# Optimization experiments

Hardware: AMD Instinct MI355X
Metric: run time of the kernel (lower is better)

## Reference

```python
import jax, jax.numpy as jnp
import numpy as np

N_NODES = 50000
N_EDGES = 800000
F_IN = 512
H1 = 64
H2 = 128
N_CLASSES = 10
N_GRAPHS = 64


def _sage_conv(x, src, dst, w_l, b_l, w_r, n_nodes):
    # mean-aggregate neighbor features (messages flow src -> dst), then
    # out = lin_l(mean_neigh) + lin_r(x)   (PyG SAGEConv defaults)
    msg = x[src]                                           # [E, F] gather
    agg = jax.ops.segment_sum(msg, dst, num_segments=n_nodes)
    deg = jax.ops.segment_sum(jnp.ones((src.shape[0], 1), x.dtype), dst,
                              num_segments=n_nodes)
    mean = agg / jnp.maximum(deg, 1.0)                     # 0 for isolated nodes
    return mean @ w_l + b_l + x @ w_r


def setup_inputs() -> dict:
    key = jax.random.key(0)
    ks = jax.random.split(key, 12)
    x = jax.random.normal(ks[0], (N_NODES, F_IN), dtype=jnp.float32)
    edge_index = jax.random.randint(ks[1], (2, N_EDGES), 0, N_NODES, dtype=jnp.int64)
    batch = jnp.sort(jax.random.randint(ks[2], (N_NODES,), 0, N_GRAPHS, dtype=jnp.int64))

    def glorot(k, fan_in, fan_out):
        s = jnp.sqrt(6.0 / (fan_in + fan_out)).astype(jnp.float32)
        return jax.random.uniform(k, (fan_in, fan_out), jnp.float32, -s, s)

    return {
        "x": x, "edge_index": edge_index, "batch": batch,
        "w1_l": glorot(ks[3], F_IN, H1), "b1_l": jnp.zeros((H1,), jnp.float32),
        "w1_r": glorot(ks[4], F_IN, H1),
        "w2_l": glorot(ks[5], H1, H2), "b2_l": jnp.zeros((H2,), jnp.float32),
        "w2_r": glorot(ks[6], H1, H2),
        "w_fc": glorot(ks[7], H2, N_CLASSES),
        "b_fc": jnp.zeros((N_CLASSES,), jnp.float32),
    }


def reference(x, edge_index, batch, w1_l, b1_l, w1_r, w2_l, b2_l, w2_r, w_fc, b_fc):
    src, dst = edge_index[0], edge_index[1]
    n = x.shape[0]
    h = jax.nn.relu(_sage_conv(x, src, dst, w1_l, b1_l, w1_r, n))
    # dropout is identity in eval mode
    h = _sage_conv(h, src, dst, w2_l, b2_l, w2_r, n)        # [N, H2]
    # global mean pool over graphs
    summed = jax.ops.segment_sum(h, batch, num_segments=N_GRAPHS)
    cnt = jax.ops.segment_sum(jnp.ones((n, 1), h.dtype), batch, num_segments=N_GRAPHS)
    pooled = summed / jnp.maximum(cnt, 1.0)                 # [G, H2]
    logits = pooled @ w_fc + b_fc                           # [G, C]
    return jax.nn.log_softmax(logits, axis=1)
```

## Files before the change

### kernel.cpp

```cpp
#include <hip/hip_runtime.h>

#define NN 50000
#define NE 800000
#define FIN 512
#define H1DIM 64
#define H2DIM 128
#define NC 10
#define NG 64
#define NRT 3125

typedef __attribute__((ext_vector_type(8))) short bf16x8;
typedef __attribute__((ext_vector_type(4))) float f32x4;

__device__ inline short f2bf(float f) {
  unsigned u = __float_as_uint(f);
  unsigned r = u + 0x7fffu + ((u >> 16) & 1u);
  return (short)(r >> 16);
}
__device__ inline float bf2f(short s) {
  return __uint_as_float(((unsigned)(unsigned short)s) << 16);
}

__global__ __launch_bounds__(256) void xbf_prep_kernel(
    const float* __restrict__ x, short* __restrict__ xbf) {
  int w = blockIdx.x * 4 + (threadIdx.x >> 6);
  int lane = threadIdx.x & 63;
  int rt = w >> 4;
  int ks = w & 15;
  int row = rt * 16 + (lane & 15);
  int k = ks * 32 + (lane >> 4) * 8;
  const float* p = x + (size_t)row * FIN + k;
  float4 v0 = *(const float4*)(p);
  float4 v1 = *(const float4*)(p + 4);
  bf16x8 o;
  o[0] = f2bf(v0.x); o[1] = f2bf(v0.y); o[2] = f2bf(v0.z); o[3] = f2bf(v0.w);
  o[4] = f2bf(v1.x); o[5] = f2bf(v1.y); o[6] = f2bf(v1.z); o[7] = f2bf(v1.w);
  *(bf16x8*)(xbf + ((size_t)w * 64 + lane) * 8) = o;
}

__global__ __launch_bounds__(256) void wbtf_prep_kernel(
    const float* __restrict__ wl, const float* __restrict__ wr,
    short* __restrict__ wbtf) {
  int w = blockIdx.x * 4 + (threadIdx.x >> 6);
  int lane = threadIdx.x & 63;
  int ni = w >> 4;
  int ks = w & 15;
  int n = ni * 16 + (lane & 15);
  int k = ks * 32 + (lane >> 4) * 8;
  bf16x8 o;
#pragma unroll
  for (int j = 0; j < 8; j++) {
    float v = (n < 64) ? wl[(size_t)(k + j) * 64 + n]
                       : wr[(size_t)(k + j) * 64 + (n - 64)];
    o[j] = f2bf(v);
  }
  *(bf16x8*)(wbtf + ((size_t)w * 64 + lane) * 8) = o;
}

__global__ __launch_bounds__(256) void gemm1_mfma_kernel(
    const short* __restrict__ xbf, const short* __restrict__ wbtf,
    short* __restrict__ xwl, float* __restrict__ xwr) {
  int w = blockIdx.x * 4 + (threadIdx.x >> 6);
  int lane = threadIdx.x & 63;
  int rt0 = w * 2;
  int rt1 = rt0 + 1;
  if (rt0 >= NRT) return;
  bool ok1 = (rt1 < NRT);
  int rt1c = ok1 ? rt1 : rt0;

  const size_t la = (size_t)lane * 8;
  const short* pa0 = xbf + (size_t)rt0 * 8192 + la;
  const short* pa1 = xbf + (size_t)rt1c * 8192 + la;
  const short* pb = wbtf + la;

  const f32x4 z = {0.f, 0.f, 0.f, 0.f};
  f32x4 acc[2][8];
#pragma unroll
  for (int mi = 0; mi < 2; mi++)
#pragma unroll
    for (int ni = 0; ni < 8; ni++) acc[mi][ni] = z;

  bf16x8 A0[2], A1[2], B0[8], B1[8];
  A0[0] = *(const bf16x8*)(pa0);
  A0[1] = *(const bf16x8*)(pa1);
#pragma unroll
  for (int ni = 0; ni < 8; ni++)
    B0[ni] = *(const bf16x8*)(pb + (size_t)ni * 8192);

#pragma unroll
  for (int ks = 0; ks < 16; ks += 2) {
    if (ks + 1 < 16) {
      A1[0] = *(const bf16x8*)(pa0 + (ks + 1) * 512);
      A1[1] = *(const bf16x8*)(pa1 + (ks + 1) * 512);
#pragma unroll
      for (int ni = 0; ni < 8; ni++)
        B1[ni] = *(const bf16x8*)(pb + (size_t)ni * 8192 + (ks + 1) * 512);
    }
#pragma unroll
    for (int mi = 0; mi < 2; mi++)
#pragma unroll
      for (int ni = 0; ni < 8; ni++)
        acc[mi][ni] = __builtin_amdgcn_mfma_f32_16x16x32_bf16(
            A0[mi], B0[ni], acc[mi][ni], 0, 0, 0);
    if (ks + 2 < 16) {
      A0[0] = *(const bf16x8*)(pa0 + (ks + 2) * 512);
      A0[1] = *(const bf16x8*)(pa1 + (ks + 2) * 512);
#pragma unroll
      for (int ni = 0; ni < 8; ni++)
        B0[ni] = *(const bf16x8*)(pb + (size_t)ni * 8192 + (ks + 2) * 512);
    }
#pragma unroll
    for (int mi = 0; mi < 2; mi++)
#pragma unroll
      for (int ni = 0; ni < 8; ni++)
        acc[mi][ni] = __builtin_amdgcn_mfma_f32_16x16x32_bf16(
            A1[mi], B1[ni], acc[mi][ni], 0, 0, 0);
  }

  int q = lane >> 4;
  int l15 = lane & 15;
#pragma unroll
  for (int mi = 0; mi < 2; mi++) {
    if (mi == 1 && !ok1) break;
    int row_base = (mi ? rt1 : rt0) * 16 + q * 4;
#pragma unroll
    for (int ni = 0; ni < 8; ni++) {
      int col = ni * 16 + l15;
      int c = col & 63;
#pragma unroll
      for (int r = 0; r < 4; r++) {
        int row = row_base + r;
        if (col < 64) xwl[(size_t)row * 64 + c] = f2bf(acc[mi][ni][r]);
        else          xwr[(size_t)row * 64 + c] = acc[mi][ni][r];
      }
    }
  }
}

__global__ __launch_bounds__(256) void hist_kernel(const int* __restrict__ dst,
                                                   int* __restrict__ cnt) {
  int i = (blockIdx.x * 256 + threadIdx.x) * 4;
  if (i < NE) {
    int4 d = *(const int4*)(dst + i);
    atomicAdd(&cnt[d.x], 1);
    atomicAdd(&cnt[d.y], 1);
    atomicAdd(&cnt[d.z], 1);
    atomicAdd(&cnt[d.w], 1);
  }
}

#define SCAN_BLOCKS 196

__global__ __launch_bounds__(256) void scan1_kernel(const int* __restrict__ cnt,
                                                    int* __restrict__ excl,
                                                    int* __restrict__ bsum) {
  __shared__ int s[256];
  int t = threadIdx.x;
  int i = blockIdx.x * 256 + t;
  int v = (i < NN) ? cnt[i] : 0;
  s[t] = v;
  __syncthreads();
  for (int off = 1; off < 256; off <<= 1) {
    int u = (t >= off) ? s[t - off] : 0;
    __syncthreads();
    s[t] += u;
    __syncthreads();
  }
  if (i < NN) excl[i] = s[t] - v;
  if (t == 255) bsum[blockIdx.x] = s[255];
}

__global__ __launch_bounds__(256) void scan2_kernel(int* __restrict__ bsum) {
  __shared__ int s[256];
  int t = threadIdx.x;
  int v = (t < SCAN_BLOCKS) ? bsum[t] : 0;
  s[t] = v;
  __syncthreads();
  for (int off = 1; off < 256; off <<= 1) {
    int u = (t >= off) ? s[t - off] : 0;
    __syncthreads();
    s[t] += u;
    __syncthreads();
  }
  bsum[t] = s[t] - v;
}

__global__ __launch_bounds__(256) void scan3_kernel(const int* __restrict__ bsum,
                                                    int* __restrict__ rowptr,
                                                    int* __restrict__ cursor) {
  int t = threadIdx.x;
  int i = blockIdx.x * 256 + t;
  if (i < NN) {
    int p = rowptr[i] + bsum[blockIdx.x];
    rowptr[i] = p;
    cursor[i] = p;
  }
  if (i == 0) rowptr[NN] = NE;
}

__global__ __launch_bounds__(256) void scatter_kernel(
    const int* __restrict__ src, const int* __restrict__ dst,
    int* __restrict__ cursor, int* __restrict__ ssrc) {
  int i = (blockIdx.x * 256 + threadIdx.x) * 4;
  if (i < NE) {
    int4 s = *(const int4*)(src + i);
    int4 d = *(const int4*)(dst + i);
    int p0 = atomicAdd(&cursor[d.x], 1); ssrc[p0] = s.x;
    int p1 = atomicAdd(&cursor[d.y], 1); ssrc[p1] = s.y;
    int p2 = atomicAdd(&cursor[d.z], 1); ssrc[p2] = s.z;
    int p3 = atomicAdd(&cursor[d.w], 1); ssrc[p3] = s.w;
  }
}

__global__ __launch_bounds__(256) void agg1_h1_kernel(
    const int* __restrict__ rowptr, const int* __restrict__ ssrc,
    const short* __restrict__ xwl, const float* __restrict__ xwr,
    const float* __restrict__ b1, short* __restrict__ h1) {
  int node = blockIdx.x * 4 + (threadIdx.x >> 6);
  if (node >= NN) return;
  int lane = threadIdx.x & 63;
  int c = lane & 7;
  int r = lane >> 3;
  int lo = rowptr[node], hi = rowptr[node + 1];
  float acc[8];
#pragma unroll
  for (int k = 0; k < 8; k++) acc[k] = 0.f;
  for (int e = lo + r; e < hi; e += 8) {
    int s = ssrc[e];
    bf16x8 v = *(const bf16x8*)(xwl + (size_t)s * 64 + c * 8);
#pragma unroll
    for (int k = 0; k < 8; k++) acc[k] += bf2f(v[k]);
  }
#pragma unroll
  for (int k = 0; k < 8; k++) {
    acc[k] += __shfl_xor(acc[k], 8);
    acc[k] += __shfl_xor(acc[k], 16);
    acc[k] += __shfl_xor(acc[k], 32);
  }
  if (r == 0) {
    float dg = fmaxf((float)(hi - lo), 1.0f);
    const float* xr = xwr + (size_t)node * 64 + c * 8;
    bf16x8 out;
#pragma unroll
    for (int k = 0; k < 8; k++) {
      float v = fmaxf(acc[k] / dg + b1[c * 8 + k] + xr[k], 0.f);
      out[k] = f2bf(v);
    }
    *(bf16x8*)(h1 + (size_t)node * 64 + c * 8) = out;
  }
}

__global__ __launch_bounds__(256) void agg2_kernel(
    const int* __restrict__ rowptr, const int* __restrict__ ssrc,
    const short* __restrict__ h1, float* __restrict__ agg2) {
  int node = blockIdx.x * 4 + (threadIdx.x >> 6);
  if (node >= NN) return;
  int lane = threadIdx.x & 63;
  int c = lane & 7;
  int r = lane >> 3;
  int lo = rowptr[node], hi = rowptr[node + 1];
  float acc[8];
#pragma unroll
  for (int k = 0; k < 8; k++) acc[k] = 0.f;
  for (int e = lo + r; e < hi; e += 8) {
    int s = ssrc[e];
    bf16x8 v = *(const bf16x8*)(h1 + (size_t)s * 64 + c * 8);
#pragma unroll
    for (int k = 0; k < 8; k++) acc[k] += bf2f(v[k]);
  }
#pragma unroll
  for (int k = 0; k < 8; k++) {
    acc[k] += __shfl_xor(acc[k], 8);
    acc[k] += __shfl_xor(acc[k], 16);
    acc[k] += __shfl_xor(acc[k], 32);
  }
  if (r == 0) {
    float* p = agg2 + (size_t)node * 64 + c * 8;
    f32x4 lo4 = {acc[0], acc[1], acc[2], acc[3]};
    f32x4 hi4 = {acc[4], acc[5], acc[6], acc[7]};
    *(f32x4*)(p) = lo4;
    *(f32x4*)(p + 4) = hi4;
  }
}

__global__ __launch_bounds__(256) void pool1_kernel(
    const int* __restrict__ batch, const float* __restrict__ agg2,
    const short* __restrict__ h1, const int* __restrict__ rowptr,
    float* __restrict__ poolA, float* __restrict__ poolB,
    float* __restrict__ poolCnt) {
  int t = threadIdx.x;
  int c = t & 15;
  int s = t >> 4;
  int n0 = blockIdx.x * 256 + s * 16;
  int n1 = n0 + 16;
  if (n1 > NN) n1 = NN;

  f32x4 aA = {0.f, 0.f, 0.f, 0.f};
  f32x4 aB = {0.f, 0.f, 0.f, 0.f};
  int cur_g = -1;
  float run = 0.f;
  for (int n = n0; n < n1; n++) {
    int g = batch[n];
    if (g != cur_g) {
      if (cur_g >= 0) {
        float* pa = poolA + (size_t)cur_g * 64 + c * 4;
        float* pb = poolB + (size_t)cur_g * 64 + c * 4;
#pragma unroll
        for (int k = 0; k < 4; k++) {
          atomicAdd(&pa[k], aA[k]);
          atomicAdd(&pb[k], aB[k]);
        }
        if (c == 0) atomicAdd(&poolCnt[cur_g], run);
      }
      cur_g = g;
      aA = (f32x4){0.f, 0.f, 0.f, 0.f};
      aB = (f32x4){0.f, 0.f, 0.f, 0.f};
      run = 0.f;
    }
    float rd = 1.0f / fmaxf((float)(rowptr[n + 1] - rowptr[n]), 1.0f);
    f32x4 a2 = *(const f32x4*)(agg2 + (size_t)n * 64 + c * 4);
    const short* hp = h1 + (size_t)n * 64 + c * 4;
#pragma unroll
    for (int k = 0; k < 4; k++) {
      aA[k] = fmaf(a2[k], rd, aA[k]);
      aB[k] += bf2f(hp[k]);
    }
    run += 1.f;
  }
  if (cur_g >= 0) {
    float* pa = poolA + (size_t)cur_g * 64 + c * 4;
    float* pb = poolB + (size_t)cur_g * 64 + c * 4;
#pragma unroll
    for (int k = 0; k < 4; k++) {
      atomicAdd(&pa[k], aA[k]);
      atomicAdd(&pb[k], aB[k]);
    }
    if (c == 0) atomicAdd(&poolCnt[cur_g], run);
  }
}

__global__ __launch_bounds__(128) void final_kernel(
    const float* __restrict__ poolA, const float* __restrict__ poolB,
    const float* __restrict__ poolCnt, const float* __restrict__ w2l,
    const float* __restrict__ w2r, const float* __restrict__ b2,
    const float* __restrict__ wfc, const float* __restrict__ bfc,
    float* __restrict__ out) {
  int g = blockIdx.x;
  int j = threadIdx.x;
  __shared__ float sp[H2DIM];
  __shared__ float sl[NC];

  float invc = 1.0f / fmaxf(poolCnt[g], 1.0f);
  float v = b2[j];
  for (int k = 0; k < 64; k++) {
    float a = poolA[g * 64 + k] * invc;
    float b = poolB[g * 64 + k] * invc;
    v = fmaf(a, w2l[k * 128 + j], v);
    v = fmaf(b, w2r[k * 128 + j], v);
  }
  sp[j] = v;
  __syncthreads();
  if (j < NC) {
    float lg = bfc[j];
    for (int k = 0; k < H2DIM; k++) lg = fmaf(sp[k], wfc[k * NC + j], lg);
    sl[j] = lg;
  }
  __syncthreads();
  if (j < NC) {
    float m = -1e30f;
    for (int k = 0; k < NC; k++) m = fmaxf(m, sl[k]);
    float s = 0.f;
    for (int k = 0; k < NC; k++) s += expf(sl[k] - m);
    out[g * NC + j] = sl[j] - m - logf(s);
  }
}

extern "C" void kernel_launch(void* const* d_in, const int* in_sizes, int n_in,
                              void* d_out, int out_size, void* d_ws,
                              size_t ws_size, hipStream_t stream) {
  const float* x   = (const float*)d_in[0];
  const int* edge  = (const int*)d_in[1];
  const int* batch = (const int*)d_in[2];
  const float* w1l = (const float*)d_in[3];
  const float* b1l = (const float*)d_in[4];
  const float* w1r = (const float*)d_in[5];
  const float* w2l = (const float*)d_in[6];
  const float* b2l = (const float*)d_in[7];
  const float* w2r = (const float*)d_in[8];
  const float* wfc = (const float*)d_in[9];
  const float* bfc = (const float*)d_in[10];
  float* out = (float*)d_out;

  const int* src = edge;
  const int* dst = edge + NE;

  const size_t NF = (size_t)NN * 64;
  int*   cnt     = (int*)d_ws;
  float* poolA   = (float*)(cnt + NN);
  float* poolB   = poolA + (size_t)NG * 64;
  float* poolCnt = poolB + (size_t)NG * 64;
  int*   cursor  = (int*)(poolCnt + NG);
  int*   rowptr  = cursor + NN;
  int*   ssrc    = rowptr + 50004;
  int*   bsum    = ssrc + NE;
  short* xbf     = (short*)(bsum + 256);
  short* xwl     = xbf + (size_t)NN * 512;
  short* h1s     = xwl + NF;
  short* wbtf    = h1s + NF;
  float* xwr     = (float*)(wbtf + 65536);
  float* agg2    = xwr + NF;

  hipMemsetAsync(cnt, 0, (NN + 2 * NG * 64 + NG) * sizeof(int), stream);

  hist_kernel<<<(NE / 4 + 255) / 256, 256, 0, stream>>>(dst, cnt);
  scan1_kernel<<<SCAN_BLOCKS, 256, 0, stream>>>(cnt, rowptr, bsum);
  scan2_kernel<<<1, 256, 0, stream>>>(bsum);
  scan3_kernel<<<SCAN_BLOCKS, 256, 0, stream>>>(bsum, rowptr, cursor);
  scatter_kernel<<<(NE / 4 + 255) / 256, 256, 0, stream>>>(src, dst, cursor, ssrc);

  xbf_prep_kernel<<<(NRT * 16) / 4, 256, 0, stream>>>(x, xbf);
  wbtf_prep_kernel<<<32, 256, 0, stream>>>(w1l, w1r, wbtf);
  gemm1_mfma_kernel<<<(NRT / 2 + 4) / 4, 256, 0, stream>>>(xbf, wbtf, xwl, xwr);

  agg1_h1_kernel<<<(NN + 3) / 4, 256, 0, stream>>>(rowptr, ssrc, xwl, xwr, b1l, h1s);
  agg2_kernel<<<(NN + 3) / 4, 256, 0, stream>>>(rowptr, ssrc, h1s, agg2);
  pool1_kernel<<<SCAN_BLOCKS, 256, 0, stream>>>(batch, agg2, h1s, rowptr, poolA, poolB, poolCnt);
  final_kernel<<<NG, 128, 0, stream>>>(poolA, poolB, poolCnt, w2l, w2r, b2l, wfc, bfc, out);
}
```

Measured before the change: 366.5 us.

## Fuse CSR build into one grid-barrier kernel and convert x to bf16 inside GEMM

Replaces the hist/scan1/scan2/scan3/scatter launches with a single persistent sort kernel of 196 blocks. Its phases are separated by an atomic-counter grid barrier, and it zeroes the counts itself instead of relying on the memset. The separate x-to-bf16 prep pass is removed: the GEMM now loads fp32 x directly and converts in registers, and each wave handles one row tile instead of two. This saves several launches and one full read/write of the bf16 copy of x, but the grid barrier depends on all 196 blocks being co-resident, and the GEMM reads twice as many bytes of A per tile.

```diff
diff --git a/kernel.cpp b/kernel.cpp
--- a/kernel.cpp
+++ b/kernel.cpp
@@ -8,6 +8,8 @@
 #define NC 10
 #define NG 64
 #define NRT 3125
+#define SB 196
+#define SORT_THREADS (SB * 256)
 
 typedef __attribute__((ext_vector_type(8))) short bf16x8;
 typedef __attribute__((ext_vector_type(4))) float f32x4;
@@ -21,21 +23,79 @@
   return __uint_as_float(((unsigned)(unsigned short)s) << 16);
 }
 
-__global__ __launch_bounds__(256) void xbf_prep_kernel(
-    const float* __restrict__ x, short* __restrict__ xbf) {
-  int w = blockIdx.x * 4 + (threadIdx.x >> 6);
-  int lane = threadIdx.x & 63;
-  int rt = w >> 4;
-  int ks = w & 15;
-  int row = rt * 16 + (lane & 15);
-  int k = ks * 32 + (lane >> 4) * 8;
-  const float* p = x + (size_t)row * FIN + k;
-  float4 v0 = *(const float4*)(p);
-  float4 v1 = *(const float4*)(p + 4);
-  bf16x8 o;
-  o[0] = f2bf(v0.x); o[1] = f2bf(v0.y); o[2] = f2bf(v0.z); o[3] = f2bf(v0.w);
-  o[4] = f2bf(v1.x); o[5] = f2bf(v1.y); o[6] = f2bf(v1.z); o[7] = f2bf(v1.w);
-  *(bf16x8*)(xbf + ((size_t)w * 64 + lane) * 8) = o;
+__device__ __forceinline__ void gbar(int* bar, int id) {
+  __syncthreads();
+  if (threadIdx.x == 0) {
+    __threadfence();
+    atomicAdd(&bar[id], 1);
+    while (atomicAdd(&bar[id], 0) < SB) {}
+  }
+  __syncthreads();
+}
+
+__global__ __launch_bounds__(256) void sort_kernel(
+    const int* __restrict__ src, const int* __restrict__ dst,
+    int* __restrict__ cnt, int* __restrict__ rowptr, int* __restrict__ cursor,
+    int* __restrict__ bsum, int* __restrict__ ssrc, int* __restrict__ bar) {
+  const int b = blockIdx.x;
+  const int t = threadIdx.x;
+  const int idx = b * 256 + t;
+  __shared__ int s[256];
+
+  {
+    int i = ((b + 98) % SB) * 256 + t;
+    if (i < NN) cnt[i] = 0;
+  }
+  gbar(bar, 0);
+
+  for (int j = idx; j < NE / 4; j += SORT_THREADS) {
+    int4 d = *(const int4*)(dst + j * 4);
+    atomicAdd(&cnt[d.x], 1);
+    atomicAdd(&cnt[d.y], 1);
+    atomicAdd(&cnt[d.z], 1);
+    atomicAdd(&cnt[d.w], 1);
+  }
+  gbar(bar, 1);
+
+  int v = (idx < NN) ? atomicAdd(&cnt[idx], 0) : 0;
+  s[t] = v;
+  __syncthreads();
+  for (int off = 1; off < 256; off <<= 1) {
+    int u = (t >= off) ? s[t - off] : 0;
+    __syncthreads();
+    s[t] += u;
+    __syncthreads();
+  }
+  if (idx < NN) rowptr[idx] = s[t] - v;
+  if (t == 255) bsum[b] = s[255];
+  gbar(bar, 2);
+
+  int bv = (t < SB) ? atomicAdd(&bsum[t], 0) : 0;
+  s[t] = bv;
+  __syncthreads();
+  for (int off = 1; off < 256; off <<= 1) {
+    int u = (t >= off) ? s[t - off] : 0;
+    __syncthreads();
+    s[t] += u;
+    __syncthreads();
+  }
+  int prefix = (b == 0) ? 0 : s[b - 1];
+  if (idx < NN) {
+    int p = rowptr[idx] + prefix;
+    rowptr[idx] = p;
+    cursor[idx] = p;
+  }
+  if (idx == 0) rowptr[NN] = NE;
+  gbar(bar, 3);
+
+  for (int j = idx; j < NE / 4; j += SORT_THREADS) {
+    int4 sv = *(const int4*)(src + j * 4);
+    int4 dv = *(const int4*)(dst + j * 4);
+    int p0 = atomicAdd(&cursor[dv.x], 1); ssrc[p0] = sv.x;
+    int p1 = atomicAdd(&cursor[dv.y], 1); ssrc[p1] = sv.y;
+    int p2 = atomicAdd(&cursor[dv.z], 1); ssrc[p2] = sv.z;
+    int p3 = atomicAdd(&cursor[dv.w], 1); ssrc[p3] = sv.w;
+  }
 }
 
 __global__ __launch_bounds__(256) void wbtf_prep_kernel(
@@ -57,32 +117,26 @@
   *(bf16x8*)(wbtf + ((size_t)w * 64 + lane) * 8) = o;
 }
 
-__global__ __launch_bounds__(256) void gemm1_mfma_kernel(
-    const short* __restrict__ xbf, const short* __restrict__ wbtf,
+__global__ __launch_bounds__(256) void gemm1_kernel(
+    const float* __restrict__ x, const short* __restrict__ wbtf,
     short* __restrict__ xwl, float* __restrict__ xwr) {
   int w = blockIdx.x * 4 + (threadIdx.x >> 6);
+  if (w >= NRT) return;
   int lane = threadIdx.x & 63;
-  int rt0 = w * 2;
-  int rt1 = rt0 + 1;
-  if (rt0 >= NRT) return;
-  bool ok1 = (rt1 < NRT);
-  int rt1c = ok1 ? rt1 : rt0;
-
-  const size_t la = (size_t)lane * 8;
-  const short* pa0 = xbf + (size_t)rt0 * 8192 + la;
-  const short* pa1 = xbf + (size_t)rt1c * 8192 + la;
-  const short* pb = wbtf + la;
+  int l15 = lane & 15;
+  int q = lane >> 4;
+  const float* px = x + (size_t)(w * 16 + l15) * FIN + q * 8;
+  const short* pb = wbtf + (size_t)lane * 8;
 
   const f32x4 z = {0.f, 0.f, 0.f, 0.f};
-  f32x4 acc[2][8];
-#pragma unroll
-  for (int mi = 0; mi < 2; mi++)
-#pragma unroll
-    for (int ni = 0; ni < 8; ni++) acc[mi][ni] = z;
-
-  bf16x8 A0[2], A1[2], B0[8], B1[8];
-  A0[0] = *(const bf16x8*)(pa0);
-  A0[1] = *(const bf16x8*)(pa1);
+  f32x4 acc[8];
+#pragma unroll
+  for (int ni = 0; ni < 8; ni++) acc[ni] = z;
+
+  float4 av0, av1, nv0, nv1;
+  bf16x8 B0[8], B1[8];
+  av0 = *(const float4*)(px);
+  av1 = *(const float4*)(px + 4);
 #pragma unroll
   for (int ni = 0; ni < 8; ni++)
     B0[ni] = *(const bf16x8*)(pb + (size_t)ni * 8192);
@@ -90,125 +144,52 @@
 #pragma unroll
   for (int ks = 0; ks < 16; ks += 2) {
     if (ks + 1 < 16) {
-      A1[0] = *(const bf16x8*)(pa0 + (ks + 1) * 512);
-      A1[1] = *(const bf16x8*)(pa1 + (ks + 1) * 512);
+      nv0 = *(const float4*)(px + (ks + 1) * 32);
+      nv1 = *(const float4*)(px + (ks + 1) * 32 + 4);
 #pragma unroll
       for (int ni = 0; ni < 8; ni++)
         B1[ni] = *(const bf16x8*)(pb + (size_t)ni * 8192 + (ks + 1) * 512);
     }
-#pragma unroll
-    for (int mi = 0; mi < 2; mi++)
+    {
+      bf16x8 af;
+      af[0] = f2bf(av0.x); af[1] = f2bf(av0.y);
+      af[2] = f2bf(av0.z); af[3] = f2bf(av0.w);
+      af[4] = f2bf(av1.x); af[5] = f2bf(av1.y);
+      af[6] = f2bf(av1.z); af[7] = f2bf(av1.w);
 #pragma unroll
       for (int ni = 0; ni < 8; ni++)
-        acc[mi][ni] = __builtin_amdgcn_mfma_f32_16x16x32_bf16(
-            A0[mi], B0[ni], acc[mi][ni], 0, 0, 0);
+        acc[ni] = __builtin_amdgcn_mfma_f32_16x16x32_bf16(af, B0[ni], acc[ni], 0, 0, 0);
+    }
     if (ks + 2 < 16) {
-      A0[0] = *(const bf16x8*)(pa0 + (ks + 2) * 512);
-      A0[1] = *(const bf16x8*)(pa1 + (ks + 2) * 512);
+      av0 = *(const float4*)(px + (ks + 2) * 32);
+      av1 = *(const float4*)(px + (ks + 2) * 32 + 4);
 #pragma unroll
       for (int ni = 0; ni < 8; ni++)
         B0[ni] = *(const bf16x8*)(pb + (size_t)ni * 8192 + (ks + 2) * 512);
     }
-#pragma unroll
-    for (int mi = 0; mi < 2; mi++)
+    {
+      bf16x8 af;
+      af[0] = f2bf(nv0.x); af[1] = f2bf(nv0.y);
+      af[2] = f2bf(nv0.z); af[3] = f2bf(nv0.w);
+      af[4] = f2bf(nv1.x); af[5] = f2bf(nv1.y);
+      af[6] = f2bf(nv1.z); af[7] = f2bf(nv1.w);
 #pragma unroll
       for (int ni = 0; ni < 8; ni++)
-        acc[mi][ni] = __builtin_amdgcn_mfma_f32_16x16x32_bf16(
-            A1[mi], B1[ni], acc[mi][ni], 0, 0, 0);
-  }
-
-  int q = lane >> 4;
-  int l15 = lane & 15;
-#pragma unroll
-  for (int mi = 0; mi < 2; mi++) {
-    if (mi == 1 && !ok1) break;
-    int row_base = (mi ? rt1 : rt0) * 16 + q * 4;
-#pragma unroll
-    for (int ni = 0; ni < 8; ni++) {
-      int col = ni * 16 + l15;
-      int c = col & 63;
-#pragma unroll
-      for (int r = 0; r < 4; r++) {
-        int row = row_base + r;
-        if (col < 64) xwl[(size_t)row * 64 + c] = f2bf(acc[mi][ni][r]);
-        else          xwr[(size_t)row * 64 + c] = acc[mi][ni][r];
-      }
-    }
-  }
-}
-
-__global__ __launch_bounds__(256) void hist_kernel(const int* __restrict__ dst,
-                                                   int* __restrict__ cnt) {
-  int i = (blockIdx.x * 256 + threadIdx.x) * 4;
-  if (i < NE) {
-    int4 d = *(const int4*)(dst + i);
-    atomicAdd(&cnt[d.x], 1);
-    atomicAdd(&cnt[d.y], 1);
-    atomicAdd(&cnt[d.z], 1);
-    atomicAdd(&cnt[d.w], 1);
-  }
-}
-
-#define SCAN_BLOCKS 196
-
-__global__ __launch_bounds__(256) void scan1_kernel(const int* __restrict__ cnt,
-                                                    int* __restrict__ excl,
-                                                    int* __restrict__ bsum) {
-  __shared__ int s[256];
-  int t = threadIdx.x;
-  int i = blockIdx.x * 256 + t;
-  int v = (i < NN) ? cnt[i] : 0;
-  s[t] = v;
-  __syncthreads();
-  for (int off = 1; off < 256; off <<= 1) {
-    int u = (t >= off) ? s[t - off] : 0;
-    __syncthreads();
-    s[t] += u;
-    __syncthreads();
-  }
-  if (i < NN) excl[i] = s[t] - v;
-  if (t == 255) bsum[blockIdx.x] = s[255];
-}
-
-__global__ __launch_bounds__(256) void scan2_kernel(int* __restrict__ bsum) {
-  __shared__ int s[256];
-  int t = threadIdx.x;
-  int v = (t < SCAN_BLOCKS) ? bsum[t] : 0;
-  s[t] = v;
-  __syncthreads();
-  for (int off = 1; off < 256; off <<= 1) {
-    int u = (t >= off) ? s[t - off] : 0;
-    __syncthreads();
-    s[t] += u;
-    __syncthreads();
-  }
-  bsum[t] = s[t] - v;
-}
-
-__global__ __launch_bounds__(256) void scan3_kernel(const int* __restrict__ bsum,
-                                                    int* __restrict__ rowptr,
-                                                    int* __restrict__ cursor) {
-  int t = threadIdx.x;
-  int i = blockIdx.x * 256 + t;
-  if (i < NN) {
-    int p = rowptr[i] + bsum[blockIdx.x];
-    rowptr[i] = p;
-    cursor[i] = p;
-  }
-  if (i == 0) rowptr[NN] = NE;
-}
-
-__global__ __launch_bounds__(256) void scatter_kernel(
-    const int* __restrict__ src, const int* __restrict__ dst,
-    int* __restrict__ cursor, int* __restrict__ ssrc) {
-  int i = (blockIdx.x * 256 + threadIdx.x) * 4;
-  if (i < NE) {
-    int4 s = *(const int4*)(src + i);
-    int4 d = *(const int4*)(dst + i);
-    int p0 = atomicAdd(&cursor[d.x], 1); ssrc[p0] = s.x;
-    int p1 = atomicAdd(&cursor[d.y], 1); ssrc[p1] = s.y;
-    int p2 = atomicAdd(&cursor[d.z], 1); ssrc[p2] = s.z;
-    int p3 = atomicAdd(&cursor[d.w], 1); ssrc[p3] = s.w;
+        acc[ni] = __builtin_amdgcn_mfma_f32_16x16x32_bf16(af, B1[ni], acc[ni], 0, 0, 0);
+    }
+  }
+
+  int row_base = w * 16 + q * 4;
+#pragma unroll
+  for (int ni = 0; ni < 8; ni++) {
+    int col = ni * 16 + l15;
+    int c = col & 63;
+#pragma unroll
+    for (int r = 0; r < 4; r++) {
+      int row = row_base + r;
+      if (col < 64) xwl[(size_t)row * 64 + c] = f2bf(acc[ni][r]);
+      else          xwr[(size_t)row * 64 + c] = acc[ni][r];
+    }
   }
 }
 
@@ -395,35 +376,29 @@
   const int* dst = edge + NE;
 
   const size_t NF = (size_t)NN * 64;
-  int*   cnt     = (int*)d_ws;
-  float* poolA   = (float*)(cnt + NN);
+  int*   bar     = (int*)d_ws;
+  float* poolA   = (float*)(bar + 8);
   float* poolB   = poolA + (size_t)NG * 64;
   float* poolCnt = poolB + (size_t)NG * 64;
-  int*   cursor  = (int*)(poolCnt + NG);
+  int*   cnt     = (int*)(poolCnt + NG);
+  int*   cursor  = cnt + NN;
   int*   rowptr  = cursor + NN;
-  int*   ssrc    = rowptr + 50004;
-  int*   bsum    = ssrc + NE;
-  short* xbf     = (short*)(bsum + 256);
-  short* xwl     = xbf + (size_t)NN * 512;
+  int*   bsum    = rowptr + 50004;
+  int*   ssrc    = bsum + 256;
+  short* xwl     = (short*)(ssrc + NE);
   short* h1s     = xwl + NF;
   short* wbtf    = h1s + NF;
   float* xwr     = (float*)(wbtf + 65536);
   float* agg2    = xwr + NF;
 
-  hipMemsetAsync(cnt, 0, (NN + 2 * NG * 64 + NG) * sizeof(int), stream);
-
-  hist_kernel<<<(NE / 4 + 255) / 256, 256, 0, stream>>>(dst, cnt);
-  scan1_kernel<<<SCAN_BLOCKS, 256, 0, stream>>>(cnt, rowptr, bsum);
-  scan2_kernel<<<1, 256, 0, stream>>>(bsum);
-  scan3_kernel<<<SCAN_BLOCKS, 256, 0, stream>>>(bsum, rowptr, cursor);
-  scatter_kernel<<<(NE / 4 + 255) / 256, 256, 0, stream>>>(src, dst, cursor, ssrc);
-
-  xbf_prep_kernel<<<(NRT * 16) / 4, 256, 0, stream>>>(x, xbf);
+  hipMemsetAsync(bar, 0, (8 + 2 * NG * 64 + NG) * sizeof(int), stream);
+
   wbtf_prep_kernel<<<32, 256, 0, stream>>>(w1l, w1r, wbtf);
-  gemm1_mfma_kernel<<<(NRT / 2 + 4) / 4, 256, 0, stream>>>(xbf, wbtf, xwl, xwr);
+  sort_kernel<<<SB, 256, 0, stream>>>(src, dst, cnt, rowptr, cursor, bsum, ssrc, bar);
+  gemm1_kernel<<<(NRT + 3) / 4, 256, 0, stream>>>(x, wbtf, xwl, xwr);
 
   agg1_h1_kernel<<<(NN + 3) / 4, 256, 0, stream>>>(rowptr, ssrc, xwl, xwr, b1l, h1s);
   agg2_kernel<<<(NN + 3) / 4, 256, 0, stream>>>(rowptr, ssrc, h1s, agg2);
-  pool1_kernel<<<SCAN_BLOCKS, 256, 0, stream>>>(batch, agg2, h1s, rowptr, poolA, poolB, poolCnt);
+  pool1_kernel<<<SB, 256, 0, stream>>>(batch, agg2, h1s, rowptr, poolA, poolB, poolCnt);
   final_kernel<<<NG, 128, 0, stream>>>(poolA, poolB, poolCnt, w2l, w2r, b2l, wfc, bfc, out);
 }
```

New measurement: 414.0 us. 1.13x slower.
